# Kernel tuning notes

Hardware: AMD Instinct MI355X
Metric: run time of the kernel (lower is better)

## Reference

```python
import jax, jax.numpy as jnp
import numpy as np

# Problem dims
M, K, N = 16384, 1024, 1024
# QuantParams baked as constants (Python scalars in the original module)
INPUT_SCALE, INPUT_ZP = 0.05, 3
WEIGHT_SCALE, WEIGHT_ZP = 0.02, 0
OUTPUT_SCALE, OUTPUT_ZP = 0.1, -5
QMIN, QMAX = -128, 127
# round(combined_scale * 1024) computed in Python, exactly as in the torch module
SCALE_INT = round(INPUT_SCALE * WEIGHT_SCALE / OUTPUT_SCALE * 1024)  # = 10


def setup_inputs() -> dict:
    key = jax.random.key(0)
    k1, k2, k3 = jax.random.split(key, 3)
    x = jax.random.randint(k1, (M, K), -128, 128, dtype=jnp.int32).astype(jnp.int8)
    weight_int = jax.random.randint(k2, (N, K), -128, 128, dtype=jnp.int32).astype(jnp.int8)
    bias_int = jax.random.randint(k3, (N,), -1000, 1000, dtype=jnp.int32)
    return {"x": x, "weight_int": weight_int, "bias_int": bias_int}


def reference(x, weight_int, bias_int):
    # F.linear(x.int32 - input_zp, W.int32 - weight_zp, bias_int)
    xi = x.astype(jnp.int32) - INPUT_ZP            # [M, K] int32
    wi = weight_int.astype(jnp.int32) - WEIGHT_ZP  # [N, K] int32
    acc = jnp.matmul(xi, wi.T) + bias_int          # [M, N] int32 accumulate
    # integer requant: (acc * scale_int) // 1024 in int64 (torch // is floor div,
    # matching jnp floor_divide semantics)
    res = (acc.astype(jnp.int64) * SCALE_INT) // 1024
    res = jnp.clip(res + OUTPUT_ZP, QMIN, QMAX)
    return res.astype(jnp.int8)
```

## Files before the change

### kernel.cpp

```cpp
#include <hip/hip_runtime.h>
#include <stdint.h>

#define M_DIM 16384
#define N_DIM 1024
#define K_DIM 1024

#define BM 128
#define BN 128
#define BK 64
#define NKT (K_DIM / BK)
#define TILE_BYTES (BM * BK)

using i32x4 = __attribute__((ext_vector_type(4))) int;

__device__ __forceinline__ int pack4(int4 v) {
    return (v.x & 0xFF) | ((v.y & 0xFF) << 8) | ((v.z & 0xFF) << 16) | ((v.w & 0xFF) << 24);
}


__global__ __launch_bounds__(256) void pack_x_kernel(const int* __restrict__ X,
                                                     int8_t* __restrict__ xqT) {
    int mtile = blockIdx.x >> 4;
    int kt = blockIdx.x & 15;
    int8_t* outT = xqT + (size_t)blockIdx.x * TILE_BYTES;
    int tid = threadIdx.x;
#pragma unroll
    for (int i = 0; i < 2; ++i) {
        int c = i * 256 + tid;
        int row = c >> 2;
        int sig = c & 3;
        const int* src = X + ((size_t)(mtile * BM + row)) * K_DIM + kt * BK + sig * 16;
        int4 p;
        p.x = pack4(*(const int4*)(src + 0));
        p.y = pack4(*(const int4*)(src + 4));
        p.z = pack4(*(const int4*)(src + 8));
        p.w = pack4(*(const int4*)(src + 12));
        int s = sig ^ ((row >> 1) & 3);
        *(int4*)(outT + ((size_t)row * 4 + s) * 16) = p;
    }
}

__global__ __launch_bounds__(256) void pack_w_corr_kernel(const int* __restrict__ w,
                                                          const int* __restrict__ bias,
                                                          int8_t* __restrict__ wqT,
                                                          int* __restrict__ corr) {
    int n = blockIdx.x;
    int t = threadIdx.x;
    int4 v = ((const int4*)(w + (size_t)n * K_DIM))[t];
    int pk = pack4(v);
    int kt = t >> 4;
    int sig = (t >> 2) & 3;
    int d = t & 3;
    int rowin = n & 127;
    int ntile = n >> 7;
    int s = sig ^ ((rowin >> 1) & 3);
    ((int*)(wqT + ((size_t)(ntile * NKT + kt)) * TILE_BYTES))[(rowin * 4 + s) * 4 + d] = pk;

    int sum = v.x + v.y + v.z + v.w;
#pragma unroll
    for (int m = 1; m < 64; m <<= 1) sum += __shfl_xor(sum, m);
    __shared__ int partial[4];
    if ((t & 63) == 0) partial[t >> 6] = sum;
    __syncthreads();
    if (t == 0)
        corr[n] = bias[n] - 3 * (partial[0] + partial[1] + partial[2] + partial[3]);
}

__global__ __launch_bounds__(256) void gemm_kernel(const int8_t* __restrict__ xqT,
                                                   const int8_t* __restrict__ wqT,
                                                   const int* __restrict__ corr,
                                                   int* __restrict__ out) {
    __shared__ int8_t Asm[3][TILE_BYTES];
    __shared__ int8_t Bsm[3][TILE_BYTES];

    int bid = blockIdx.x;
    int swz = (bid & 7) * 128 + (bid >> 3);
    int mtile = swz >> 3;
    int ntile = swz & 7;
    int n0 = ntile * BN;

    int tid = threadIdx.x;
    int lane = tid & 63;
    int wave = tid >> 6;
    int wm = wave >> 1;
    int wn = wave & 1;
    int r16 = lane & 15;
    int krow = lane >> 4;
    int slot = krow ^ ((r16 >> 1) & 3);

    i32x4 acc[4][4];
#pragma unroll
    for (int i = 0; i < 4; ++i)
#pragma unroll
        for (int j = 0; j < 4; ++j)
            acc[i][j] = (i32x4){0, 0, 0, 0};

    const int8_t* Abase = xqT + (size_t)mtile * NKT * TILE_BYTES;
    const int8_t* Bbase = wqT + (size_t)ntile * NKT * TILE_BYTES;

#define STAGE(buf, kt)                                                                     \
    {                                                                                      \
        const int8_t* Ag = Abase + (size_t)(kt) * TILE_BYTES;                              \
        const int8_t* Bg = Bbase + (size_t)(kt) * TILE_BYTES;                              \
        _Pragma("unroll") for (int i = 0; i < 2; ++i) {                                    \
            int f = i * 256 + tid;                                                         \
            __builtin_amdgcn_global_load_lds(                                              \
                (const __attribute__((address_space(1))) unsigned int*)(Ag + (size_t)f * 16), \
                (__attribute__((address_space(3))) unsigned int*)(&Asm[buf][0] + f * 16),  \
                16, 0, 0);                                                                 \
        }                                                                                  \
        _Pragma("unroll") for (int i = 0; i < 2; ++i) {                                    \
            int f = i * 256 + tid;                                                         \
            __builtin_amdgcn_global_load_lds(                                              \
                (const __attribute__((address_space(1))) unsigned int*)(Bg + (size_t)f * 16), \
                (__attribute__((address_space(3))) unsigned int*)(&Bsm[buf][0] + f * 16),  \
                16, 0, 0);                                                                 \
        }                                                                                  \
    }

    STAGE(0, 0);
    STAGE(1, 1);

#pragma unroll
    for (int kt = 0; kt < NKT; ++kt) {
        const int cur = kt % 3;
        if (kt < NKT - 2) {
            STAGE((kt + 2) % 3, kt + 2);
            asm volatile("s_waitcnt vmcnt(8)" ::: "memory");
        } else if (kt == NKT - 2) {
            asm volatile("s_waitcnt vmcnt(4)" ::: "memory");
        } else {
            asm volatile("s_waitcnt vmcnt(0)" ::: "memory");
        }
        __builtin_amdgcn_s_barrier();

        i32x4 afr[4], bfr[4];
#pragma unroll
        for (int i = 0; i < 4; ++i) {
            afr[i] = *(const i32x4*)(&Asm[cur][0] + (size_t)(wm * 64 + i * 16 + r16) * 64 + slot * 16);
            bfr[i] = *(const i32x4*)(&Bsm[cur][0] + (size_t)(wn * 64 + i * 16 + r16) * 64 + slot * 16);
        }
#pragma unroll
        for (int i = 0; i < 4; ++i)
#pragma unroll
            for (int j = 0; j < 4; ++j)
                acc[i][j] = __builtin_amdgcn_mfma_i32_16x16x64_i8(afr[i], bfr[j], acc[i][j], 0, 0, 0);

        if (kt < NKT - 1) __builtin_amdgcn_s_barrier();
    }
#undef STAGE

    int m0 = mtile * BM;
    int col16 = lane & 15;
    int rbase = (lane >> 4) * 4;
    int cr[4];
#pragma unroll
    for (int j = 0; j < 4; ++j) cr[j] = corr[n0 + wn * 64 + j * 16 + col16];
#pragma unroll
    for (int i = 0; i < 4; ++i) {
        int rrow = m0 + wm * 64 + i * 16 + rbase;
#pragma unroll
        for (int r = 0; r < 4; ++r) {
            size_t rowoff = (size_t)(rrow + r) * N_DIM;
#pragma unroll
            for (int j = 0; j < 4; ++j) {
                int t = acc[i][j][r] + cr[j];
                int res = ((t * 10) >> 10) - 5;
                res = res < -128 ? -128 : (res > 127 ? 127 : res);
                out[rowoff + n0 + wn * 64 + j * 16 + col16] = res;
            }
        }
    }
}

extern "C" void kernel_launch(void* const* d_in, const int* in_sizes, int n_in,
                              void* d_out, int out_size, void* d_ws, size_t ws_size,
                              hipStream_t stream) {
    (void)in_sizes; (void)n_in; (void)out_size; (void)ws_size;
    const int* x    = (const int*)d_in[0];
    const int* w    = (const int*)d_in[1];
    const int* bias = (const int*)d_in[2];
    int* out = (int*)d_out;

    int8_t* xqT = (int8_t*)d_ws;
    int8_t* wqT = xqT + (size_t)M_DIM * K_DIM;
    int* corr   = (int*)(wqT + (size_t)N_DIM * K_DIM);

    pack_x_kernel<<<(M_DIM / BM) * NKT, 256, 0, stream>>>(x, xqT);
    pack_w_corr_kernel<<<N_DIM, 256, 0, stream>>>(w, bias, wqT, corr);
    gemm_kernel<<<(M_DIM / BM) * (N_DIM / BN), 256, 0, stream>>>(xqT, wqT, corr, out);
}
```

Before: 138.1 us.

## Fuse X int8 packing into GEMM A-tile loading via registers

Removes the separate pack_x kernel and instead loads int32 X directly in the GEMM, packing to int8 in registers and writing swizzled tiles into LDS, with B still loaded via global_load_lds. The goal is to avoid the intermediate int8 X buffer's write and re-read and one kernel launch. In exchange, each of the 8 N-tile blocks per M-tile re-reads the 4-byte int32 X from global memory, and the pipeline gains register staging plus rewritten waitcnt/barrier scheduling.

```diff
diff --git a/kernel.cpp b/kernel.cpp
--- a/kernel.cpp
+++ b/kernel.cpp
@@ -14,31 +14,9 @@
 using i32x4 = __attribute__((ext_vector_type(4))) int;
 
 __device__ __forceinline__ int pack4(int4 v) {
-    return (v.x & 0xFF) | ((v.y & 0xFF) << 8) | ((v.z & 0xFF) << 16) | ((v.w & 0xFF) << 24);
+    return (v.x & 0xFF) | ((v.y & 0xFF) << 8) | ((v.z & 0xFF) << 16) | (v.w << 24);
 }
 
-
-__global__ __launch_bounds__(256) void pack_x_kernel(const int* __restrict__ X,
-                                                     int8_t* __restrict__ xqT) {
-    int mtile = blockIdx.x >> 4;
-    int kt = blockIdx.x & 15;
-    int8_t* outT = xqT + (size_t)blockIdx.x * TILE_BYTES;
-    int tid = threadIdx.x;
-#pragma unroll
-    for (int i = 0; i < 2; ++i) {
-        int c = i * 256 + tid;
-        int row = c >> 2;
-        int sig = c & 3;
-        const int* src = X + ((size_t)(mtile * BM + row)) * K_DIM + kt * BK + sig * 16;
-        int4 p;
-        p.x = pack4(*(const int4*)(src + 0));
-        p.y = pack4(*(const int4*)(src + 4));
-        p.z = pack4(*(const int4*)(src + 8));
-        p.w = pack4(*(const int4*)(src + 12));
-        int s = sig ^ ((row >> 1) & 3);
-        *(int4*)(outT + ((size_t)row * 4 + s) * 16) = p;
-    }
-}
 
 __global__ __launch_bounds__(256) void pack_w_corr_kernel(const int* __restrict__ w,
                                                           const int* __restrict__ bias,
@@ -66,10 +44,10 @@
         corr[n] = bias[n] - 3 * (partial[0] + partial[1] + partial[2] + partial[3]);
 }
 
-__global__ __launch_bounds__(256) void gemm_kernel(const int8_t* __restrict__ xqT,
-                                                   const int8_t* __restrict__ wqT,
-                                                   const int* __restrict__ corr,
-                                                   int* __restrict__ out) {
+__global__ __launch_bounds__(256) void gemm_fused_kernel(const int* __restrict__ X,
+                                                         const int8_t* __restrict__ wqT,
+                                                         const int* __restrict__ corr,
+                                                         int* __restrict__ out) {
     __shared__ int8_t Asm[3][TILE_BYTES];
     __shared__ int8_t Bsm[3][TILE_BYTES];
 
@@ -78,6 +56,7 @@
     int mtile = swz >> 3;
     int ntile = swz & 7;
     int n0 = ntile * BN;
+    int m0 = mtile * BM;
 
     int tid = threadIdx.x;
     int lane = tid & 63;
@@ -95,44 +74,61 @@
         for (int j = 0; j < 4; ++j)
             acc[i][j] = (i32x4){0, 0, 0, 0};
 
-    const int8_t* Abase = xqT + (size_t)mtile * NKT * TILE_BYTES;
+    int arow[2], asig[2];
+    const int* Abase[2];
+#pragma unroll
+    for (int g = 0; g < 2; ++g) {
+        int c = g * 256 + tid;
+        arow[g] = c >> 2;
+        asig[g] = c & 3;
+        Abase[g] = X + (size_t)(m0 + arow[g]) * K_DIM + asig[g] * 16;
+    }
     const int8_t* Bbase = wqT + (size_t)ntile * NKT * TILE_BYTES;
 
-#define STAGE(buf, kt)                                                                     \
-    {                                                                                      \
-        const int8_t* Ag = Abase + (size_t)(kt) * TILE_BYTES;                              \
-        const int8_t* Bg = Bbase + (size_t)(kt) * TILE_BYTES;                              \
-        _Pragma("unroll") for (int i = 0; i < 2; ++i) {                                    \
-            int f = i * 256 + tid;                                                         \
-            __builtin_amdgcn_global_load_lds(                                              \
-                (const __attribute__((address_space(1))) unsigned int*)(Ag + (size_t)f * 16), \
-                (__attribute__((address_space(3))) unsigned int*)(&Asm[buf][0] + f * 16),  \
-                16, 0, 0);                                                                 \
-        }                                                                                  \
-        _Pragma("unroll") for (int i = 0; i < 2; ++i) {                                    \
-            int f = i * 256 + tid;                                                         \
-            __builtin_amdgcn_global_load_lds(                                              \
+    int4 areg[2][4];
+
+#define ALD(kt)                                                                        \
+    {                                                                                  \
+        _Pragma("unroll") for (int g = 0; g < 2; ++g)                                  \
+            _Pragma("unroll") for (int q = 0; q < 4; ++q)                              \
+                areg[g][q] = *(const int4*)(Abase[g] + (size_t)(kt) * BK + q * 4);     \
+    }
+
+#define APW(buf)                                                                       \
+    {                                                                                  \
+        _Pragma("unroll") for (int g = 0; g < 2; ++g) {                                \
+            i32x4 p;                                                                   \
+            p[0] = pack4(areg[g][0]);                                                  \
+            p[1] = pack4(areg[g][1]);                                                  \
+            p[2] = pack4(areg[g][2]);                                                  \
+            p[3] = pack4(areg[g][3]);                                                  \
+            int su = asig[g] ^ ((arow[g] >> 1) & 3);                                   \
+            *(i32x4*)(&Asm[buf][0] + ((size_t)arow[g] * 4 + su) * 16) = p;             \
+        }                                                                              \
+    }
+
+#define BST(buf, kt)                                                                   \
+    {                                                                                  \
+        const int8_t* Bg = Bbase + (size_t)(kt) * TILE_BYTES;                          \
+        _Pragma("unroll") for (int i = 0; i < 2; ++i) {                                \
+            int f = i * 256 + tid;                                                     \
+            __builtin_amdgcn_global_load_lds(                                          \
                 (const __attribute__((address_space(1))) unsigned int*)(Bg + (size_t)f * 16), \
                 (__attribute__((address_space(3))) unsigned int*)(&Bsm[buf][0] + f * 16),  \
-                16, 0, 0);                                                                 \
-        }                                                                                  \
+                16, 0, 0);                                                             \
+        }                                                                              \
     }
 
-    STAGE(0, 0);
-    STAGE(1, 1);
+    ALD(0); BST(0, 0);
+    asm volatile("s_waitcnt vmcnt(2)" ::: "memory");
+    APW(0);
+    ALD(1); BST(1, 1);
+    asm volatile("s_waitcnt vmcnt(10) lgkmcnt(0)" ::: "memory");
+    __builtin_amdgcn_s_barrier();
 
 #pragma unroll
     for (int kt = 0; kt < NKT; ++kt) {
         const int cur = kt % 3;
-        if (kt < NKT - 2) {
-            STAGE((kt + 2) % 3, kt + 2);
-            asm volatile("s_waitcnt vmcnt(8)" ::: "memory");
-        } else if (kt == NKT - 2) {
-            asm volatile("s_waitcnt vmcnt(4)" ::: "memory");
-        } else {
-            asm volatile("s_waitcnt vmcnt(0)" ::: "memory");
-        }
-        __builtin_amdgcn_s_barrier();
 
         i32x4 afr[4], bfr[4];
 #pragma unroll
@@ -146,11 +142,22 @@
             for (int j = 0; j < 4; ++j)
                 acc[i][j] = __builtin_amdgcn_mfma_i32_16x16x64_i8(afr[i], bfr[j], acc[i][j], 0, 0, 0);
 
-        if (kt < NKT - 1) __builtin_amdgcn_s_barrier();
+        if (kt <= NKT - 2) {
+            asm volatile("s_waitcnt vmcnt(2)" ::: "memory");
+            APW((kt + 1) % 3);
+            if (kt <= NKT - 3) {
+                ALD(kt + 2); BST((kt + 2) % 3, kt + 2);
+                asm volatile("s_waitcnt vmcnt(10) lgkmcnt(0)" ::: "memory");
+            } else {
+                asm volatile("s_waitcnt vmcnt(0) lgkmcnt(0)" ::: "memory");
+            }
+            __builtin_amdgcn_s_barrier();
+        }
     }
-#undef STAGE
+#undef ALD
+#undef APW
+#undef BST
 
-    int m0 = mtile * BM;
     int col16 = lane & 15;
     int rbase = (lane >> 4) * 4;
     int cr[4];
@@ -182,11 +189,9 @@
     const int* bias = (const int*)d_in[2];
     int* out = (int*)d_out;
 
-    int8_t* xqT = (int8_t*)d_ws;
-    int8_t* wqT = xqT + (size_t)M_DIM * K_DIM;
+    int8_t* wqT = (int8_t*)d_ws;
     int* corr   = (int*)(wqT + (size_t)N_DIM * K_DIM);
 
-    pack_x_kernel<<<(M_DIM / BM) * NKT, 256, 0, stream>>>(x, xqT);
     pack_w_corr_kernel<<<N_DIM, 256, 0, stream>>>(w, bias, wqT, corr);
-    gemm_kernel<<<(M_DIM / BM) * (N_DIM / BN), 256, 0, stream>>>(xqT, wqT, corr, out);
+    gemm_fused_kernel<<<(M_DIM / BM) * (N_DIM / BN), 256, 0, stream>>>(x, wqT, corr, out);
 }
```

Measured after the change: 167.2 us. 1.21x slower.
